# Performance work log

Measured on AMD Instinct MI355X. Metric: run time of the kernel, lower is better.

## Reference

```python
import jax, jax.numpy as jnp
import numpy as np


def setup_inputs() -> dict:
    key = jax.random.key(0)
    k1, k2, k3, k4 = jax.random.split(key, 4)
    B, T, D, L = 32, 30, 512, 196
    x = jax.random.normal(k1, (B, T, D), dtype=jnp.float32)
    wordemb = jax.random.normal(k2, (B, T, D), dtype=jnp.float32)
    imgsfeats = jax.random.normal(k3, (B, L, D), dtype=jnp.float32)
    v_w = jax.random.normal(k4, (D,), dtype=jnp.float32) * (1.0 / np.sqrt(D))
    v_b = jnp.zeros((1,), dtype=jnp.float32)
    return {"x": x, "wordemb": wordemb, "imgsfeats": imgsfeats, "v_w": v_w, "v_b": v_b}


def reference(x, wordemb, imgsfeats, v_w, v_b):
    # x, wordemb: (B, T=30, D=512); imgsfeats: (B, L, D)
    # y = imgsfeats.transpose(2,1) broadcast over T: (B, 1, D, L)
    y = jnp.transpose(imgsfeats, (0, 2, 1))[:, None, :, :]          # (B,1,D,L)
    att = jnp.tanh(x[:, :, :, None] + y + wordemb[:, :, :, None])   # (B,T,D,L)
    # score: linear D->1 applied along D
    e = jnp.einsum('btdl,d->btl', att, v_w) + v_b[0]                 # (B,T,L)
    alpha = jax.nn.softmax(e, axis=-1)                               # (B,T,L)
    # context = sum_l y * alpha -> (B,T,D)
    context = jnp.einsum('bld,btl->btd', imgsfeats, alpha)
    return context
```

## Files before the change

kernel.cpp:

```cpp
#include <hip/hip_runtime.h>

namespace {
constexpr int kB = 32, kT = 30, kD = 512, kL = 196;
constexpr float kK = 2.8853900817779268f;
constexpr size_t kGsz = (size_t)kB * kT * kL;

#define PAIR(ex, ey, fx, fy, vx, vy, acc)                                   \
  {                                                                         \
    const float u_ = fmaf(ex, fx, 1.f);                                     \
    const float v_ = fmaf(ey, fy, 1.f);                                     \
    acc = fmaf(fmaf(v_, vx, u_ * vy), __builtin_amdgcn_rcpf(u_ * v_), acc); \
  }

__global__ __launch_bounds__(512) void k_score(const float* __restrict__ x,
                                               const float* __restrict__ w,
                                               const float* __restrict__ img,
                                               const float* __restrict__ vw,
                                               float* __restrict__ g8) {
  __shared__ __align__(16) float4 Fl4[16 * 64];
  __shared__ __align__(16) float4 El4[32 * 16];
  __shared__ __align__(16) float4 vwl4[16];
  int n = blockIdx.x;
  const int bg = n & 7;
  int m = n >> 3;
  const int bi = m & 3; m >>= 2;
  const int lc = m % 3;
  const int dqg = m / 3;
  const int b = bg * 4 + bi;
  const int l0 = lc * 64, d0 = dqg * 64;
  const int tid = threadIdx.x;
  {
    const int l = tid >> 3, c0 = tid & 7;
#pragma unroll
    for (int k = 0; k < 2; ++k) {
      const int c = c0 + 8 * k;
      const float4 v =
          *(const float4*)(img + ((size_t)(b * kL + l0 + l)) * kD + d0 + 4 * c);
      float4 o;
      o.x = __builtin_amdgcn_exp2f(kK * v.x);
      o.y = __builtin_amdgcn_exp2f(kK * v.y);
      o.z = __builtin_amdgcn_exp2f(kK * v.z);
      o.w = __builtin_amdgcn_exp2f(kK * v.w);
      Fl4[c * 64 + (l ^ (c & 7))] = o;
    }
  }
  {
    const int row = tid >> 4, c4 = tid & 15;
    const int tc = (row < kT) ? row : kT - 1;
    const size_t gi = ((size_t)(b * kT + tc)) * kD + d0 + 4 * c4;
    const float4 xv = *(const float4*)(x + gi);
    const float4 wv4 = *(const float4*)(w + gi);
    float4 e;
    e.x = __builtin_amdgcn_exp2f(kK * (xv.x + wv4.x));
    e.y = __builtin_amdgcn_exp2f(kK * (xv.y + wv4.y));
    e.z = __builtin_amdgcn_exp2f(kK * (xv.z + wv4.z));
    e.w = __builtin_amdgcn_exp2f(kK * (xv.w + wv4.w));
    El4[row * 16 + c4] = e;
  }
  if (tid < 16) vwl4[tid] = *(const float4*)(vw + d0 + 4 * tid);
  __syncthreads();
  const int lane = tid & 63, wva = tid >> 6;
  const int r0 = wva * 4;
  const float4* Ew = &El4[r0 * 16];
  float a0 = 0.f, a1 = 0.f, a2 = 0.f, a3 = 0.f;
#pragma unroll
  for (int s = 0; s < 16; ++s) {
    const float4 f = Fl4[s * 64 + (lane ^ (s & 7))];
    const float4 vv = vwl4[s];
    const float4 E0 = Ew[s];
    const float4 E1 = Ew[16 + s];
    const float4 E2 = Ew[32 + s];
    const float4 E3 = Ew[48 + s];
    PAIR(E0.x, E0.y, f.x, f.y, vv.x, vv.y, a0);
    PAIR(E0.z, E0.w, f.z, f.w, vv.z, vv.w, a0);
    PAIR(E1.x, E1.y, f.x, f.y, vv.x, vv.y, a1);
    PAIR(E1.z, E1.w, f.z, f.w, vv.z, vv.w, a1);
    PAIR(E2.x, E2.y, f.x, f.y, vv.x, vv.y, a2);
    PAIR(E2.z, E2.w, f.z, f.w, vv.z, vv.w, a2);
    PAIR(E3.x, E3.y, f.x, f.y, vv.x, vv.y, a3);
    PAIR(E3.z, E3.w, f.z, f.w, vv.z, vv.w, a3);
  }
  float* gp =
      g8 + (size_t)dqg * kGsz + ((size_t)(b * kT + r0)) * kL + l0 + lane;
  gp[0] = a0;
  gp[kL] = a1;
  if (r0 + 2 < kT) gp[2 * kL] = a2;
  if (r0 + 3 < kT) gp[3 * kL] = a3;
}

__global__ __launch_bounds__(512) void k_alpha(const float* __restrict__ g8,
                                               const float* __restrict__ x,
                                               const float* __restrict__ w,
                                               const float* __restrict__ img,
                                               const float* __restrict__ vw,
                                               float* __restrict__ alpha) {
  const int qd = blockIdx.x, b = blockIdx.y;
  const int lane = threadIdx.x & 63, wv = threadIdx.x >> 6;
  const int t = qd * 8 + wv;
  if (t >= kT) return;
  const int l4 = lane & 3, dc = lane >> 2;
  const float* ir = img + ((size_t)(b * kL + 192 + l4)) * kD + dc * 32;
  const float* xr = x + ((size_t)(b * kT + t)) * kD + dc * 32;
  const float* wr = w + ((size_t)(b * kT + t)) * kD + dc * 32;
  const float* vr = vw + dc * 32;
  float tg = 0.f;
#pragma unroll
  for (int k = 0; k < 8; ++k) {
    const float4 iv = *(const float4*)(ir + 4 * k);
    const float4 xv = *(const float4*)(xr + 4 * k);
    const float4 wv4 = *(const float4*)(wr + 4 * k);
    const float4 vv = *(const float4*)(vr + 4 * k);
    const float fx = __builtin_amdgcn_exp2f(kK * iv.x);
    const float fy = __builtin_amdgcn_exp2f(kK * iv.y);
    const float fz = __builtin_amdgcn_exp2f(kK * iv.z);
    const float fw = __builtin_amdgcn_exp2f(kK * iv.w);
    const float ex = __builtin_amdgcn_exp2f(kK * (xv.x + wv4.x));
    const float ey = __builtin_amdgcn_exp2f(kK * (xv.y + wv4.y));
    const float ez = __builtin_amdgcn_exp2f(kK * (xv.z + wv4.z));
    const float ew = __builtin_amdgcn_exp2f(kK * (xv.w + wv4.w));
    PAIR(ex, ey, fx, fy, vv.x, vv.y, tg);
    PAIR(ez, ew, fz, fw, vv.z, vv.w, tg);
  }
#pragma unroll
  for (int mm = 4; mm < 64; mm <<= 1) tg += __shfl_xor(tg, mm, 64);
  const size_t base = ((size_t)(b * kT + t)) * kL;
  float q0 = 0.f, q1 = 0.f, q2 = 0.f;
#pragma unroll
  for (int p = 0; p < 8; ++p) {
    const float* gp = g8 + (size_t)p * kGsz + base;
    q0 += gp[lane];
    q1 += gp[lane + 64];
    q2 += gp[lane + 128];
  }
  q0 *= kK; q1 *= kK; q2 *= kK;
  float q3 = (lane < 4) ? tg * kK : __builtin_inff();
  float m = fminf(fminf(q0, q1), fminf(q2, q3));
#pragma unroll
  for (int mm = 1; mm < 64; mm <<= 1) m = fminf(m, __shfl_xor(m, mm, 64));
  const float e0 = __builtin_amdgcn_exp2f(m - q0);
  const float e1 = __builtin_amdgcn_exp2f(m - q1);
  const float e2 = __builtin_amdgcn_exp2f(m - q2);
  const float e3 = (lane < 4) ? __builtin_amdgcn_exp2f(m - q3) : 0.f;
  float s = e0 + e1 + e2 + e3;
#pragma unroll
  for (int mm = 1; mm < 64; mm <<= 1) s += __shfl_xor(s, mm, 64);
  const float rs = __builtin_amdgcn_rcpf(s);
  float* ab = alpha + base;
  ab[lane] = e0 * rs;
  ab[lane + 64] = e1 * rs;
  ab[lane + 128] = e2 * rs;
  if (lane < 4) ab[lane + 192] = e3 * rs;
}

__global__ __launch_bounds__(256) void k_ctx(const float* __restrict__ img,
                                             const float* __restrict__ alpha,
                                             float* __restrict__ out) {
  __shared__ __align__(16) float red[4][5][256];
  int n = blockIdx.x;
  const int bg = n & 7;
  int m = n >> 3;
  const int bi = m & 3; m >>= 2;
  const int tg = m % 6;
  const int dh = m / 6;
  const int b = bg * 4 + bi;
  const int t0 = tg * 5, d0 = dh * 256;
  const int tid = threadIdx.x;
  const int lane = tid & 63;
  const int lru = __builtin_amdgcn_readfirstlane(tid >> 6);
  const float* ap = alpha + ((size_t)(b * kT + t0)) * kL + lru * 49;
  const float* ip = img + ((size_t)(b * kL + lru * 49)) * kD + d0 + 4 * lane;
  float4 acc[5];
#pragma unroll
  for (int j = 0; j < 5; ++j) acc[j] = {0.f, 0.f, 0.f, 0.f};
  auto loadI = [&](float4* dst, int bb) {
#pragma unroll
    for (int j = 0; j < 8; ++j)
      dst[j] = *(const float4*)(ip + (size_t)(bb * 8 + j) * kD);
  };
  auto compI = [&](const float4* f, int bb) {
#pragma unroll
    for (int j = 0; j < 8; ++j) {
      const int i = bb * 8 + j;
      const float a0 = ap[i];
      const float a1 = ap[kL + i];
      const float a2 = ap[2 * kL + i];
      const float a3 = ap[3 * kL + i];
      const float a4 = ap[4 * kL + i];
      acc[0].x = fmaf(f[j].x, a0, acc[0].x); acc[0].y = fmaf(f[j].y, a0, acc[0].y);
      acc[0].z = fmaf(f[j].z, a0, acc[0].z); acc[0].w = fmaf(f[j].w, a0, acc[0].w);
      acc[1].x = fmaf(f[j].x, a1, acc[1].x); acc[1].y = fmaf(f[j].y, a1, acc[1].y);
      acc[1].z = fmaf(f[j].z, a1, acc[1].z); acc[1].w = fmaf(f[j].w, a1, acc[1].w);
      acc[2].x = fmaf(f[j].x, a2, acc[2].x); acc[2].y = fmaf(f[j].y, a2, acc[2].y);
      acc[2].z = fmaf(f[j].z, a2, acc[2].z); acc[2].w = fmaf(f[j].w, a2, acc[2].w);
      acc[3].x = fmaf(f[j].x, a3, acc[3].x); acc[3].y = fmaf(f[j].y, a3, acc[3].y);
      acc[3].z = fmaf(f[j].z, a3, acc[3].z); acc[3].w = fmaf(f[j].w, a3, acc[3].w);
      acc[4].x = fmaf(f[j].x, a4, acc[4].x); acc[4].y = fmaf(f[j].y, a4, acc[4].y);
      acc[4].z = fmaf(f[j].z, a4, acc[4].z); acc[4].w = fmaf(f[j].w, a4, acc[4].w);
    }
  };
  float4 fA[8], fB[8];
  loadI(fA, 0);
  loadI(fB, 1); compI(fA, 0);
  loadI(fA, 2); compI(fB, 1);
  loadI(fB, 3); compI(fA, 2);
  loadI(fA, 4); compI(fB, 3);
  loadI(fB, 5); compI(fA, 4);
  compI(fB, 5);
  {
    const float4 v = *(const float4*)(ip + (size_t)48 * kD);
    const int i = 48;
    const float a0 = ap[i], a1 = ap[kL + i], a2 = ap[2 * kL + i],
                a3 = ap[3 * kL + i], a4 = ap[4 * kL + i];
    acc[0].x = fmaf(v.x, a0, acc[0].x); acc[0].y = fmaf(v.y, a0, acc[0].y);
    acc[0].z = fmaf(v.z, a0, acc[0].z); acc[0].w = fmaf(v.w, a0, acc[0].w);
    acc[1].x = fmaf(v.x, a1, acc[1].x); acc[1].y = fmaf(v.y, a1, acc[1].y);
    acc[1].z = fmaf(v.z, a1, acc[1].z); acc[1].w = fmaf(v.w, a1, acc[1].w);
    acc[2].x = fmaf(v.x, a2, acc[2].x); acc[2].y = fmaf(v.y, a2, acc[2].y);
    acc[2].z = fmaf(v.z, a2, acc[2].z); acc[2].w = fmaf(v.w, a2, acc[2].w);
    acc[3].x = fmaf(v.x, a3, acc[3].x); acc[3].y = fmaf(v.y, a3, acc[3].y);
    acc[3].z = fmaf(v.z, a3, acc[3].z); acc[3].w = fmaf(v.w, a3, acc[3].w);
    acc[4].x = fmaf(v.x, a4, acc[4].x); acc[4].y = fmaf(v.y, a4, acc[4].y);
    acc[4].z = fmaf(v.z, a4, acc[4].z); acc[4].w = fmaf(v.w, a4, acc[4].w);
  }
#pragma unroll
  for (int j = 0; j < 5; ++j) *(float4*)&red[lru][j][4 * lane] = acc[j];
  __syncthreads();
#pragma unroll
  for (int j = 0; j < 5; ++j) {
    const float s =
        red[0][j][tid] + red[1][j][tid] + red[2][j][tid] + red[3][j][tid];
    out[((size_t)(b * kT + t0 + j)) * kD + d0 + tid] = s;
  }
}
}

extern "C" void kernel_launch(void* const* d_in, const int* in_sizes, int n_in,
                              void* d_out, int out_size, void* d_ws, size_t ws_size,
                              hipStream_t stream) {
  const float* x = (const float*)d_in[0];
  const float* wordemb = (const float*)d_in[1];
  const float* img = (const float*)d_in[2];
  const float* vw = (const float*)d_in[3];
  float* out = (float*)d_out;
  float* g8 = (float*)d_ws;
  float* alpha = g8 + 8 * kGsz;
  hipLaunchKernelGGL(k_score, dim3(768), dim3(512), 0, stream, x, wordemb, img,
                     vw, g8);
  hipLaunchKernelGGL(k_alpha, dim3(4, kB), dim3(512), 0, stream, g8, x, wordemb,
                     img, vw, alpha);
  hipLaunchKernelGGL(k_ctx, dim3(384), dim3(256), 0, stream, img, alpha, out);
}
```

Baseline: 33.48 us.

## Split score D-chunk across wave halves with 8 rows per wave and LDS reduction

Each wave now computes 8 time rows over half of the 64-wide D chunk instead of 4 rows over the full chunk. Partial sums from the second half are combined through a new shared-memory buffer and a second barrier before the global store. The image load loop is also re-indexed so consecutive threads read consecutive float4s along D. This is meant to reuse each loaded F value across more rows and give better coalescing, at the cost of extra LDS traffic, a sync, and more accumulator registers.

```diff
diff --git a/kernel.cpp b/kernel.cpp
--- a/kernel.cpp
+++ b/kernel.cpp
@@ -20,6 +20,7 @@
   __shared__ __align__(16) float4 Fl4[16 * 64];
   __shared__ __align__(16) float4 El4[32 * 16];
   __shared__ __align__(16) float4 vwl4[16];
+  __shared__ __align__(16) float sc[4 * 8 * 64];
   int n = blockIdx.x;
   const int bg = n & 7;
   int m = n >> 3;
@@ -29,20 +30,18 @@
   const int b = bg * 4 + bi;
   const int l0 = lc * 64, d0 = dqg * 64;
   const int tid = threadIdx.x;
-  {
-    const int l = tid >> 3, c0 = tid & 7;
-#pragma unroll
-    for (int k = 0; k < 2; ++k) {
-      const int c = c0 + 8 * k;
-      const float4 v =
-          *(const float4*)(img + ((size_t)(b * kL + l0 + l)) * kD + d0 + 4 * c);
-      float4 o;
-      o.x = __builtin_amdgcn_exp2f(kK * v.x);
-      o.y = __builtin_amdgcn_exp2f(kK * v.y);
-      o.z = __builtin_amdgcn_exp2f(kK * v.z);
-      o.w = __builtin_amdgcn_exp2f(kK * v.w);
-      Fl4[c * 64 + (l ^ (c & 7))] = o;
-    }
+#pragma unroll
+  for (int k = 0; k < 2; ++k) {
+    const int i = tid + k * 512;
+    const int l = i >> 4, c = i & 15;
+    const float4 v =
+        *(const float4*)(img + ((size_t)(b * kL + l0 + l)) * kD + d0 + 4 * c);
+    float4 o;
+    o.x = __builtin_amdgcn_exp2f(kK * v.x);
+    o.y = __builtin_amdgcn_exp2f(kK * v.y);
+    o.z = __builtin_amdgcn_exp2f(kK * v.z);
+    o.w = __builtin_amdgcn_exp2f(kK * v.w);
+    Fl4[c * 64 + (l ^ (c & 7))] = o;
   }
   {
     const int row = tid >> 4, c4 = tid & 15;
@@ -60,32 +59,39 @@
   if (tid < 16) vwl4[tid] = *(const float4*)(vw + d0 + 4 * tid);
   __syncthreads();
   const int lane = tid & 63, wva = tid >> 6;
-  const int r0 = wva * 4;
+  const int tg = wva & 3, dh = wva >> 2;
+  const int r0 = tg * 8;
   const float4* Ew = &El4[r0 * 16];
-  float a0 = 0.f, a1 = 0.f, a2 = 0.f, a3 = 0.f;
-#pragma unroll
-  for (int s = 0; s < 16; ++s) {
-    const float4 f = Fl4[s * 64 + (lane ^ (s & 7))];
-    const float4 vv = vwl4[s];
-    const float4 E0 = Ew[s];
-    const float4 E1 = Ew[16 + s];
-    const float4 E2 = Ew[32 + s];
-    const float4 E3 = Ew[48 + s];
-    PAIR(E0.x, E0.y, f.x, f.y, vv.x, vv.y, a0);
-    PAIR(E0.z, E0.w, f.z, f.w, vv.z, vv.w, a0);
-    PAIR(E1.x, E1.y, f.x, f.y, vv.x, vv.y, a1);
-    PAIR(E1.z, E1.w, f.z, f.w, vv.z, vv.w, a1);
-    PAIR(E2.x, E2.y, f.x, f.y, vv.x, vv.y, a2);
-    PAIR(E2.z, E2.w, f.z, f.w, vv.z, vv.w, a2);
-    PAIR(E3.x, E3.y, f.x, f.y, vv.x, vv.y, a3);
-    PAIR(E3.z, E3.w, f.z, f.w, vv.z, vv.w, a3);
-  }
-  float* gp =
-      g8 + (size_t)dqg * kGsz + ((size_t)(b * kT + r0)) * kL + l0 + lane;
-  gp[0] = a0;
-  gp[kL] = a1;
-  if (r0 + 2 < kT) gp[2 * kL] = a2;
-  if (r0 + 3 < kT) gp[3 * kL] = a3;
+  float acc[8];
+#pragma unroll
+  for (int tt = 0; tt < 8; ++tt) acc[tt] = 0.f;
+#pragma unroll
+  for (int s = 0; s < 8; ++s) {
+    const int c4 = dh * 8 + s;
+    const float4 f = Fl4[c4 * 64 + (lane ^ s)];
+    const float4 vv = vwl4[c4];
+#pragma unroll
+    for (int tt = 0; tt < 8; ++tt) {
+      const float4 E = Ew[tt * 16 + c4];
+      PAIR(E.x, E.y, f.x, f.y, vv.x, vv.y, acc[tt]);
+      PAIR(E.z, E.w, f.z, f.w, vv.z, vv.w, acc[tt]);
+    }
+  }
+  if (dh == 1) {
+#pragma unroll
+    for (int tt = 0; tt < 8; ++tt) sc[(tg * 8 + tt) * 64 + lane] = acc[tt];
+  }
+  __syncthreads();
+  if (dh == 0) {
+    float* gp =
+        g8 + (size_t)dqg * kGsz + ((size_t)(b * kT + r0)) * kL + l0 + lane;
+#pragma unroll
+    for (int tt = 0; tt < 8; ++tt) {
+      if (r0 + tt < kT) {
+        gp[(size_t)tt * kL] = acc[tt] + sc[(tg * 8 + tt) * 64 + lane];
+      }
+    }
+  }
 }
 
 __global__ __launch_bounds__(512) void k_alpha(const float* __restrict__ g8,
```

New measurement: 31.14 us. -7.0%, faster.
